# Kernel optimization log

Hardware: AMD Instinct MI355X
Metric: run time of the kernel (lower is better)

## Reference

```python
import math
import jax, jax.numpy as jnp
import numpy as np

IN_DIM = 128
OUT_DIM = 128
D_TIME = 64
N_SRC = 50000
N_DST = 50000
E = 800000
SCALE = math.sqrt(2 * OUT_DIM + D_TIME)  # sqrt(attn_input_dim)


def setup_inputs() -> dict:
    key = jax.random.key(0)
    k1, k2, k3, k4, k5, k6, k7 = jax.random.split(key, 7)
    h_src = jax.random.normal(k1, (N_SRC, IN_DIM), dtype=jnp.float32)
    h_dst = jax.random.normal(k2, (N_DST, IN_DIM), dtype=jnp.float32)
    edge_index = jax.random.randint(k3, (2, E), 0, N_DST, dtype=jnp.int32)
    phi_dt = jax.random.normal(k4, (E, D_TIME), dtype=jnp.float32)
    # parameters (Kaiming-ish scaling like nn.Linear defaults)
    W_src = jax.random.normal(k5, (OUT_DIM, IN_DIM), dtype=jnp.float32) / math.sqrt(IN_DIM)
    W_dst = jax.random.normal(k6, (OUT_DIM, IN_DIM), dtype=jnp.float32) / math.sqrt(IN_DIM)
    attn_w = jax.random.normal(k7, (2 * OUT_DIM + D_TIME,), dtype=jnp.float32) / math.sqrt(2 * OUT_DIM + D_TIME)
    return {"h_src": h_src, "h_dst": h_dst, "edge_index": edge_index,
            "phi_dt": phi_dt, "W_src": W_src, "W_dst": W_dst, "attn_w": attn_w}


def reference(h_src, h_dst, edge_index, phi_dt, W_src, W_dst, attn_w):
    num_dst = h_dst.shape[0]
    src_idx, dst_idx = edge_index[0], edge_index[1]
    # gather + per-edge linear projections: [E, out_dim]
    z_s = h_src[src_idx] @ W_src.T
    z_d = h_dst[dst_idx] @ W_dst.T
    # attn(cat([z_s, z_d, phi])) == z_s@a_s + z_d@a_d + phi@a_t (avoids concat)
    a_s = attn_w[:OUT_DIM]
    a_d = attn_w[OUT_DIM:2 * OUT_DIM]
    a_t = attn_w[2 * OUT_DIM:]
    e = z_s @ a_s + z_d @ a_d + phi_dt @ a_t  # [E]
    e = jax.nn.leaky_relu(e, 0.2) / SCALE
    # numerically stable segment softmax over dst neighbourhoods
    seg_max = jax.ops.segment_max(e, dst_idx, num_segments=num_dst)
    ex = jnp.exp(e - seg_max[dst_idx])
    seg_sum = jax.ops.segment_sum(ex, dst_idx, num_segments=num_dst)
    alpha = ex / (seg_sum[dst_idx] + 1e-12)
    # dropout is identity at inference
    msg = alpha[:, None] * z_s  # [E, out_dim]
    out = jax.ops.segment_sum(msg, dst_idx, num_segments=num_dst)  # [N_dst, out_dim]
    return out
```

## Files before the change

### kernel.cpp

```cpp
#include <hip/hip_runtime.h>
#include <hip/hip_bf16.h>
#include <math.h>

#define IN_DIM   128
#define OUT_DIM  128
#define D_TIME   64
#define NSRC     50000
#define NDST     50000
#define NE       800000
#define NPB      20
#define SLOTS    64
#define EPB      64
#define INV_SCALE 0.05590169943749474f

__global__ void k_prevec(const float* __restrict__ Ws, const float* __restrict__ Wd,
                         const float* __restrict__ attn,
                         float* __restrict__ v_s, float* __restrict__ v_d){
    int t = threadIdx.x;
    const float* W = (t < 128) ? Ws : Wd;
    const float* a = (t < 128) ? attn : attn + OUT_DIM;
    float* o       = (t < 128) ? v_s : v_d;
    int k = t & 127;
    float acc = 0.f;
    for (int j = 0; j < OUT_DIM; ++j) acc += W[j*IN_DIM + k] * a[j];
    o[k] = acc;
}

__global__ __launch_bounds__(128) void k_transform(const float* __restrict__ h_src,
                                                   const float* __restrict__ W,
                                                   float* __restrict__ Z){
    __shared__ float h[2][IN_DIM];
    int t = threadIdx.x;
    float4 wreg[32];
    const float4* wv = (const float4*)(W + (size_t)t * IN_DIM);
    #pragma unroll
    for (int i = 0; i < 32; ++i) wreg[i] = wv[i];
    int base = blockIdx.x * NPB;
    h[0][t] = h_src[(size_t)base*IN_DIM + t];
    for (int nn = 0; nn < NPB; ++nn){
        __syncthreads();
        if (nn + 1 < NPB) h[(nn+1)&1][t] = h_src[(size_t)(base+nn+1)*IN_DIM + t];
        const float* hc = h[nn&1];
        float acc = 0.f;
        #pragma unroll
        for (int i = 0; i < 32; ++i){
            float4 w = wreg[i]; int k = i*4;
            acc += hc[k+0]*w.x + hc[k+1]*w.y + hc[k+2]*w.z + hc[k+3]*w.w;
        }
        Z[(size_t)(base+nn)*OUT_DIM + t] = acc;
    }
}

__global__ __launch_bounds__(256) void k_dots(const float* __restrict__ h_src,
                                              const float* __restrict__ h_dst,
                                              const float* __restrict__ v_s,
                                              const float* __restrict__ v_d,
                                              float* __restrict__ s_src,
                                              float* __restrict__ s_dst){
    __shared__ float vd[IN_DIM];
    int t = threadIdx.x;
    bool isDst = (blockIdx.x >= NSRC/4);
    const float* h = isDst ? h_dst : h_src;
    const float* v = isDst ? v_d  : v_s;
    float*       s = isDst ? s_dst : s_src;
    int b = isDst ? (blockIdx.x - NSRC/4) : blockIdx.x;
    if (t < IN_DIM) vd[t] = v[t];
    __syncthreads();
    int wave = t >> 6, lane = t & 63;
    int node = b * 4 + wave;
    float2 u = ((const float2*)(h + (size_t)node*IN_DIM))[lane];
    float acc = u.x*vd[2*lane] + u.y*vd[2*lane+1];
    #pragma unroll
    for (int off = 32; off > 0; off >>= 1) acc += __shfl_down(acc, off, 64);
    if (lane == 0) s[node] = acc;
}

__global__ __launch_bounds__(256) void k_score(const float* __restrict__ phi,
                                               const float* __restrict__ attn,
                                               float* __restrict__ pt){
    __shared__ float at[D_TIME];
    int t = threadIdx.x;
    if (t < D_TIME) at[t] = attn[2*OUT_DIM + t];
    __syncthreads();
    int sub = t & 15;
    int e0 = blockIdx.x * EPB + (t >> 4);
    float a0 = at[sub*4+0], a1 = at[sub*4+1], a2 = at[sub*4+2], a3 = at[sub*4+3];
    float4 w[4];
    #pragma unroll
    for (int p = 0; p < 4; ++p)
        w[p] = ((const float4*)(phi + (size_t)(e0 + p*16) * D_TIME))[sub];
    #pragma unroll
    for (int p = 0; p < 4; ++p){
        float acc = w[p].x*a0 + w[p].y*a1 + w[p].z*a2 + w[p].w*a3;
        #pragma unroll
        for (int off = 8; off > 0; off >>= 1) acc += __shfl_xor(acc, off, 64);
        if (sub == 0) pt[e0 + p*16] = acc;
    }
}

__global__ __launch_bounds__(256) void k_slot(const int* __restrict__ ei,
                                              const float* __restrict__ pt,
                                              const float* __restrict__ s_src,
                                              const float* __restrict__ s_dst,
                                              int2* __restrict__ slots,
                                              int* __restrict__ counts){
    int e = blockIdx.x * 256 + threadIdx.x;
    int src = ei[e], dst = ei[NE + e];
    float v = s_src[src] + s_dst[dst] + pt[e];
    v = (v > 0.f) ? v : 0.2f * v;
    v *= INV_SCALE;
    int k = atomicAdd(&counts[dst], 1);
    if (k < SLOTS) slots[(dst << 6) + k] = make_int2(src, __float_as_int(v));
}

__global__ __launch_bounds__(256) void k_agg(const int* __restrict__ counts,
                                             const int2* __restrict__ slots,
                                             const float* __restrict__ Z,
                                             float* __restrict__ out){
    int wv = threadIdx.x >> 6, lane = threadIdx.x & 63;
    int d = blockIdx.x * 4 + wv;
    int cnt = counts[d]; cnt = (cnt > SLOTS) ? SLOTS : cnt;
    float e = -1e30f; int src = 0;
    if (lane < cnt){
        int2 s = slots[(d << 6) + lane];
        src = s.x; e = __int_as_float(s.y);
    }
    float m = e;
    #pragma unroll
    for (int off = 32; off > 0; off >>= 1) m = fmaxf(m, __shfl_xor(m, off, 64));
    float ex = (lane < cnt) ? __expf(e - m) : 0.f;
    float sum = ex;
    #pragma unroll
    for (int off = 32; off > 0; off >>= 1) sum += __shfl_xor(sum, off, 64);
    float alpha = ex / (sum + 1e-12f);
    float2 acc = make_float2(0.f, 0.f);
    int jmax = (cnt + 3) & ~3;
    for (int j = 0; j < jmax; j += 4){
        float a0 = __shfl(alpha, j,   64); int s0 = __shfl(src, j,   64);
        float a1 = __shfl(alpha, j+1, 64); int s1 = __shfl(src, j+1, 64);
        float a2 = __shfl(alpha, j+2, 64); int s2 = __shfl(src, j+2, 64);
        float a3 = __shfl(alpha, j+3, 64); int s3 = __shfl(src, j+3, 64);
        float2 z0 = ((const float2*)(Z + (size_t)s0 * OUT_DIM))[lane];
        float2 z1 = ((const float2*)(Z + (size_t)s1 * OUT_DIM))[lane];
        float2 z2 = ((const float2*)(Z + (size_t)s2 * OUT_DIM))[lane];
        float2 z3 = ((const float2*)(Z + (size_t)s3 * OUT_DIM))[lane];
        acc.x += a0*z0.x + a1*z1.x + a2*z2.x + a3*z3.x;
        acc.y += a0*z0.y + a1*z1.y + a2*z2.y + a3*z3.y;
    }
    ((float2*)(out + (size_t)d * OUT_DIM))[lane] = acc;
}

extern "C" void kernel_launch(void* const* d_in, const int* in_sizes, int n_in,
                              void* d_out, int out_size, void* d_ws, size_t ws_size,
                              hipStream_t stream){
    const float* h_src = (const float*)d_in[0];
    const float* h_dst = (const float*)d_in[1];
    const int*   ei    = (const int*)d_in[2];
    const float* phi   = (const float*)d_in[3];
    const float* Wsrc  = (const float*)d_in[4];
    const float* Wdst  = (const float*)d_in[5];
    const float* attn  = (const float*)d_in[6];
    float* out = (float*)d_out;

    char* p = (char*)d_ws;
    auto alloc = [&](size_t bytes)->char*{
        char* r = p; p += (bytes + 255) / 256 * 256; return r;
    };
    float* Z     = (float*)alloc((size_t)NSRC*OUT_DIM*4);
    float* s_src = (float*)alloc((size_t)NSRC*4);
    float* s_dst = (float*)alloc((size_t)NDST*4);
    float* v_s   = (float*)alloc(128*4);
    float* v_d   = (float*)alloc(128*4);
    float* pt    = (float*)alloc((size_t)NE*4);
    int2*  slots = (int2*)alloc((size_t)NDST*SLOTS*8);
    int*   counts= (int*)alloc((size_t)NDST*4);

    hipMemsetAsync(counts, 0, (size_t)NDST*4, stream);

    k_prevec<<<1, 256, 0, stream>>>(Wsrc, Wdst, attn, v_s, v_d);
    k_transform<<<NSRC/NPB, 128, 0, stream>>>(h_src, Wsrc, Z);
    k_dots<<<(NSRC + NDST)/4, 256, 0, stream>>>(h_src, h_dst, v_s, v_d, s_src, s_dst);
    k_score<<<NE/EPB, 256, 0, stream>>>(phi, attn, pt);
    k_slot<<<NE/256, 256, 0, stream>>>(ei, pt, s_src, s_dst, slots, counts);
    k_agg<<<NDST/4, 256, 0, stream>>>(counts, slots, Z, out);
}
```

Measured before the change: 523.3 us.

## Fuse pipeline into fewer kernels and store projected source features in fp16

Merges the transform and node-dot kernels into one launch and merges the time-score and slot-insertion kernels so the per-edge time score stays in shared memory. The counts memset is folded into the front kernel, and prevec is parallelised across 64 blocks with wave reductions. The projected source features Z are stored as fp16, halving gather traffic in aggregation. The cost is reduced precision in the message values, plus a heterogeneous block mix in the fused front kernel.

```diff
diff --git a/kernel.cpp b/kernel.cpp
--- a/kernel.cpp
+++ b/kernel.cpp
@@ -1,5 +1,5 @@
 #include <hip/hip_runtime.h>
-#include <hip/hip_bf16.h>
+#include <hip/hip_fp16.h>
 #include <math.h>
 
 #define IN_DIM   128
@@ -13,77 +13,92 @@
 #define EPB      64
 #define INV_SCALE 0.05590169943749474f
 
-__global__ void k_prevec(const float* __restrict__ Ws, const float* __restrict__ Wd,
-                         const float* __restrict__ attn,
-                         float* __restrict__ v_s, float* __restrict__ v_d){
-    int t = threadIdx.x;
-    const float* W = (t < 128) ? Ws : Wd;
-    const float* a = (t < 128) ? attn : attn + OUT_DIM;
-    float* o       = (t < 128) ? v_s : v_d;
-    int k = t & 127;
-    float acc = 0.f;
-    for (int j = 0; j < OUT_DIM; ++j) acc += W[j*IN_DIM + k] * a[j];
-    o[k] = acc;
+__global__ __launch_bounds__(256) void k_prevec(const float* __restrict__ Ws,
+                                                const float* __restrict__ Wd,
+                                                const float* __restrict__ attn,
+                                                float* __restrict__ v_s,
+                                                float* __restrict__ v_d){
+    int wv = threadIdx.x >> 6, lane = threadIdx.x & 63;
+    int o = blockIdx.x * 4 + wv;
+    const float* W = (o < 128) ? Ws : Wd;
+    const float* a = (o < 128) ? attn : attn + OUT_DIM;
+    float*       v = (o < 128) ? v_s : v_d;
+    int k = o & 127;
+    int j = 2 * lane;
+    float acc = W[(size_t)j*IN_DIM + k] * a[j] + W[(size_t)(j+1)*IN_DIM + k] * a[j+1];
+    #pragma unroll
+    for (int off = 32; off > 0; off >>= 1) acc += __shfl_down(acc, off, 64);
+    if (lane == 0) v[k] = acc;
 }
 
-__global__ __launch_bounds__(128) void k_transform(const float* __restrict__ h_src,
-                                                   const float* __restrict__ W,
-                                                   float* __restrict__ Z){
-    __shared__ float h[2][IN_DIM];
+__global__ __launch_bounds__(256) void k_front(const float* __restrict__ h_src,
+                                               const float* __restrict__ h_dst,
+                                               const float* __restrict__ W,
+                                               const float* __restrict__ v_s,
+                                               const float* __restrict__ v_d,
+                                               __half* __restrict__ Zh,
+                                               float* __restrict__ s_src,
+                                               float* __restrict__ s_dst,
+                                               int* __restrict__ counts){
     int t = threadIdx.x;
-    float4 wreg[32];
-    const float4* wv = (const float4*)(W + (size_t)t * IN_DIM);
-    #pragma unroll
-    for (int i = 0; i < 32; ++i) wreg[i] = wv[i];
-    int base = blockIdx.x * NPB;
-    h[0][t] = h_src[(size_t)base*IN_DIM + t];
-    for (int nn = 0; nn < NPB; ++nn){
+    if (blockIdx.x < NSRC/NPB){
+        __shared__ float h[2][2][IN_DIM];
+        int hh = t >> 7, tl = t & 127;
+        float4 wreg[32];
+        const float4* wvp = (const float4*)(W + (size_t)tl * IN_DIM);
+        #pragma unroll
+        for (int i = 0; i < 32; ++i) wreg[i] = wvp[i];
+        int base = blockIdx.x * NPB + hh * (NPB/2);
+        h[hh][0][tl] = h_src[(size_t)base*IN_DIM + tl];
+        for (int nn = 0; nn < NPB/2; ++nn){
+            __syncthreads();
+            if (nn + 1 < NPB/2) h[hh][(nn+1)&1][tl] = h_src[(size_t)(base+nn+1)*IN_DIM + tl];
+            const float* hc = h[hh][nn&1];
+            float acc = 0.f;
+            #pragma unroll
+            for (int i = 0; i < 32; ++i){
+                float4 w = wreg[i]; int k = i*4;
+                acc += hc[k+0]*w.x + hc[k+1]*w.y + hc[k+2]*w.z + hc[k+3]*w.w;
+            }
+            Zh[(size_t)(base+nn)*OUT_DIM + tl] = __float2half_rn(acc);
+        }
+    } else {
+        __shared__ float vd[IN_DIM];
+        int b = blockIdx.x - NSRC/NPB;
+        bool isDst = (b >= NSRC/4);
+        const float* h = isDst ? h_dst : h_src;
+        const float* v = isDst ? v_d  : v_s;
+        float*       s = isDst ? s_dst : s_src;
+        int bb = isDst ? (b - NSRC/4) : b;
+        if (t < IN_DIM) vd[t] = v[t];
         __syncthreads();
-        if (nn + 1 < NPB) h[(nn+1)&1][t] = h_src[(size_t)(base+nn+1)*IN_DIM + t];
-        const float* hc = h[nn&1];
-        float acc = 0.f;
+        int wave = t >> 6, lane = t & 63;
+        int node = bb * 4 + wave;
+        float2 u = ((const float2*)(h + (size_t)node*IN_DIM))[lane];
+        float acc = u.x*vd[2*lane] + u.y*vd[2*lane+1];
         #pragma unroll
-        for (int i = 0; i < 32; ++i){
-            float4 w = wreg[i]; int k = i*4;
-            acc += hc[k+0]*w.x + hc[k+1]*w.y + hc[k+2]*w.z + hc[k+3]*w.w;
+        for (int off = 32; off > 0; off >>= 1) acc += __shfl_down(acc, off, 64);
+        if (lane == 0){
+            s[node] = acc;
+            if (isDst) counts[node] = 0;
         }
-        Z[(size_t)(base+nn)*OUT_DIM + t] = acc;
     }
 }
 
-__global__ __launch_bounds__(256) void k_dots(const float* __restrict__ h_src,
-                                              const float* __restrict__ h_dst,
-                                              const float* __restrict__ v_s,
-                                              const float* __restrict__ v_d,
-                                              float* __restrict__ s_src,
-                                              float* __restrict__ s_dst){
-    __shared__ float vd[IN_DIM];
-    int t = threadIdx.x;
-    bool isDst = (blockIdx.x >= NSRC/4);
-    const float* h = isDst ? h_dst : h_src;
-    const float* v = isDst ? v_d  : v_s;
-    float*       s = isDst ? s_dst : s_src;
-    int b = isDst ? (blockIdx.x - NSRC/4) : blockIdx.x;
-    if (t < IN_DIM) vd[t] = v[t];
-    __syncthreads();
-    int wave = t >> 6, lane = t & 63;
-    int node = b * 4 + wave;
-    float2 u = ((const float2*)(h + (size_t)node*IN_DIM))[lane];
-    float acc = u.x*vd[2*lane] + u.y*vd[2*lane+1];
-    #pragma unroll
-    for (int off = 32; off > 0; off >>= 1) acc += __shfl_down(acc, off, 64);
-    if (lane == 0) s[node] = acc;
-}
-
-__global__ __launch_bounds__(256) void k_score(const float* __restrict__ phi,
-                                               const float* __restrict__ attn,
-                                               float* __restrict__ pt){
+__global__ __launch_bounds__(256) void k_edge(const float* __restrict__ phi,
+                                              const float* __restrict__ attn,
+                                              const int* __restrict__ ei,
+                                              const float* __restrict__ s_src,
+                                              const float* __restrict__ s_dst,
+                                              int2* __restrict__ slots,
+                                              int* __restrict__ counts){
     __shared__ float at[D_TIME];
+    __shared__ float pts[EPB];
     int t = threadIdx.x;
     if (t < D_TIME) at[t] = attn[2*OUT_DIM + t];
     __syncthreads();
-    int sub = t & 15;
-    int e0 = blockIdx.x * EPB + (t >> 4);
+    int sub = t & 15, g = t >> 4;
+    int e0 = blockIdx.x * EPB + g;
     float a0 = at[sub*4+0], a1 = at[sub*4+1], a2 = at[sub*4+2], a3 = at[sub*4+3];
     float4 w[4];
     #pragma unroll
@@ -94,28 +109,23 @@
         float acc = w[p].x*a0 + w[p].y*a1 + w[p].z*a2 + w[p].w*a3;
         #pragma unroll
         for (int off = 8; off > 0; off >>= 1) acc += __shfl_xor(acc, off, 64);
-        if (sub == 0) pt[e0 + p*16] = acc;
+        if (sub == 0) pts[g + p*16] = acc;
     }
-}
-
-__global__ __launch_bounds__(256) void k_slot(const int* __restrict__ ei,
-                                              const float* __restrict__ pt,
-                                              const float* __restrict__ s_src,
-                                              const float* __restrict__ s_dst,
-                                              int2* __restrict__ slots,
-                                              int* __restrict__ counts){
-    int e = blockIdx.x * 256 + threadIdx.x;
-    int src = ei[e], dst = ei[NE + e];
-    float v = s_src[src] + s_dst[dst] + pt[e];
-    v = (v > 0.f) ? v : 0.2f * v;
-    v *= INV_SCALE;
-    int k = atomicAdd(&counts[dst], 1);
-    if (k < SLOTS) slots[(dst << 6) + k] = make_int2(src, __float_as_int(v));
+    __syncthreads();
+    if (t < EPB){
+        int e = blockIdx.x * EPB + t;
+        int src = ei[e], dst = ei[NE + e];
+        float v = s_src[src] + s_dst[dst] + pts[t];
+        v = (v > 0.f) ? v : 0.2f * v;
+        v *= INV_SCALE;
+        int k = atomicAdd(&counts[dst], 1);
+        if (k < SLOTS) slots[(dst << 6) + k] = make_int2(src, __float_as_int(v));
+    }
 }
 
 __global__ __launch_bounds__(256) void k_agg(const int* __restrict__ counts,
                                              const int2* __restrict__ slots,
-                                             const float* __restrict__ Z,
+                                             const __half* __restrict__ Zh,
                                              float* __restrict__ out){
     int wv = threadIdx.x >> 6, lane = threadIdx.x & 63;
     int d = blockIdx.x * 4 + wv;
@@ -140,12 +150,16 @@
         float a1 = __shfl(alpha, j+1, 64); int s1 = __shfl(src, j+1, 64);
         float a2 = __shfl(alpha, j+2, 64); int s2 = __shfl(src, j+2, 64);
         float a3 = __shfl(alpha, j+3, 64); int s3 = __shfl(src, j+3, 64);
-        float2 z0 = ((const float2*)(Z + (size_t)s0 * OUT_DIM))[lane];
-        float2 z1 = ((const float2*)(Z + (size_t)s1 * OUT_DIM))[lane];
-        float2 z2 = ((const float2*)(Z + (size_t)s2 * OUT_DIM))[lane];
-        float2 z3 = ((const float2*)(Z + (size_t)s3 * OUT_DIM))[lane];
-        acc.x += a0*z0.x + a1*z1.x + a2*z2.x + a3*z3.x;
-        acc.y += a0*z0.y + a1*z1.y + a2*z2.y + a3*z3.y;
+        __half2 z0 = ((const __half2*)(Zh + (size_t)s0 * OUT_DIM))[lane];
+        __half2 z1 = ((const __half2*)(Zh + (size_t)s1 * OUT_DIM))[lane];
+        __half2 z2 = ((const __half2*)(Zh + (size_t)s2 * OUT_DIM))[lane];
+        __half2 z3 = ((const __half2*)(Zh + (size_t)s3 * OUT_DIM))[lane];
+        float2 f0 = __half22float2(z0);
+        float2 f1 = __half22float2(z1);
+        float2 f2 = __half22float2(z2);
+        float2 f3 = __half22float2(z3);
+        acc.x += a0*f0.x + a1*f1.x + a2*f2.x + a3*f3.x;
+        acc.y += a0*f0.y + a1*f1.y + a2*f2.y + a3*f3.y;
     }
     ((float2*)(out + (size_t)d * OUT_DIM))[lane] = acc;
 }
@@ -166,21 +180,17 @@
     auto alloc = [&](size_t bytes)->char*{
         char* r = p; p += (bytes + 255) / 256 * 256; return r;
     };
-    float* Z     = (float*)alloc((size_t)NSRC*OUT_DIM*4);
+    __half* Zh   = (__half*)alloc((size_t)NSRC*OUT_DIM*2);
     float* s_src = (float*)alloc((size_t)NSRC*4);
     float* s_dst = (float*)alloc((size_t)NDST*4);
     float* v_s   = (float*)alloc(128*4);
     float* v_d   = (float*)alloc(128*4);
-    float* pt    = (float*)alloc((size_t)NE*4);
     int2*  slots = (int2*)alloc((size_t)NDST*SLOTS*8);
     int*   counts= (int*)alloc((size_t)NDST*4);
 
-    hipMemsetAsync(counts, 0, (size_t)NDST*4, stream);
-
-    k_prevec<<<1, 256, 0, stream>>>(Wsrc, Wdst, attn, v_s, v_d);
-    k_transform<<<NSRC/NPB, 128, 0, stream>>>(h_src, Wsrc, Z);
-    k_dots<<<(NSRC + NDST)/4, 256, 0, stream>>>(h_src, h_dst, v_s, v_d, s_src, s_dst);
-    k_score<<<NE/EPB, 256, 0, stream>>>(phi, attn, pt);
-    k_slot<<<NE/256, 256, 0, stream>>>(ei, pt, s_src, s_dst, slots, counts);
-    k_agg<<<NDST/4, 256, 0, stream>>>(counts, slots, Z, out);
+    k_prevec<<<64, 256, 0, stream>>>(Wsrc, Wdst, attn, v_s, v_d);
+    k_front<<<NSRC/NPB + (NSRC + NDST)/4, 256, 0, stream>>>(
+        h_src, h_dst, Wsrc, v_s, v_d, Zh, s_src, s_dst, counts);
+    k_edge<<<NE/EPB, 256, 0, stream>>>(phi, attn, ei, s_src, s_dst, slots, counts);
+    k_agg<<<NDST/4, 256, 0, stream>>>(counts, slots, Zh, out);
 }
```

New measurement: 477.9 us. -8.7%, faster.
